# Kernel tuning notes

Hardware: AMD Instinct MI355X
Metric: run time of the kernel (lower is better)

## Reference

```python
import jax, jax.numpy as jnp
import numpy as np

B, C, H, W = 4, 256, 160, 160
N = 512
REID = 128
NUM_LAYERS = 2
BINS = 7          # adaptive_avg_pool2d target (7,7)
EPS_BN = 1e-5
EPS_NORM = 1e-12  # torch F.normalize eps


def setup_inputs() -> dict:
    key = jax.random.key(0)
    ks = jax.random.split(key, 8)
    x = jax.random.normal(ks[0], (B, C, H, W), jnp.float32)
    # valid normalized boxes: x1,y1 in [0,0.7], w,h in [0.1,0.3]
    xy1 = jax.random.uniform(ks[1], (B, N, 2), minval=0.0, maxval=0.7)
    wh = jax.random.uniform(ks[2], (B, N, 2), minval=0.1, maxval=0.3)
    bboxes = jnp.concatenate([xy1, jnp.minimum(xy1 + wh, 1.0)], axis=-1)
    # conv stack params (kaiming-ish init), BN in eval mode with running stats
    conv_w = jax.random.normal(ks[3], (NUM_LAYERS, C, C, 3, 3), jnp.float32) * np.sqrt(2.0 / (C * 9)).astype(np.float32)
    conv_b = jnp.zeros((NUM_LAYERS, C), jnp.float32)
    bn_gamma = jnp.ones((NUM_LAYERS, C), jnp.float32)
    bn_beta = jnp.zeros((NUM_LAYERS, C), jnp.float32)
    bn_mean = jnp.zeros((NUM_LAYERS, C), jnp.float32)
    bn_var = jnp.ones((NUM_LAYERS, C), jnp.float32)
    # reid_embedding MLP: Linear(C, C//2) -> ReLU -> Dropout(eval) -> Linear(C//2, REID)
    w1 = jax.random.normal(ks[4], (C // 2, C), jnp.float32) * 0.01
    b1 = jnp.zeros((C // 2,), jnp.float32)
    w2 = jax.random.normal(ks[5], (REID, C // 2), jnp.float32) * 0.01
    b2 = jnp.zeros((REID,), jnp.float32)
    return dict(x=x, bboxes=bboxes, conv_w=conv_w, conv_b=conv_b,
                bn_gamma=bn_gamma, bn_beta=bn_beta, bn_mean=bn_mean, bn_var=bn_var,
                w1=w1, b1=b1, w2=w2, b2=b2)


def _conv_bn_relu(x, w, b, gamma, beta, mean, var):
    y = jax.lax.conv_general_dilated(
        x, w, window_strides=(1, 1), padding=((1, 1), (1, 1)),
        dimension_numbers=('NCHW', 'OIHW', 'NCHW')) + b[None, :, None, None]
    scale = (gamma / jnp.sqrt(var + EPS_BN))[None, :, None, None]
    y = (y - mean[None, :, None, None]) * scale + beta[None, :, None, None]
    return jax.nn.relu(y)


def _roi_pool(S, box):
    # S: (C, H+1, W+1) integral image of the feature map; box: (4,) = x1,y1,x2,y2 in [0,1]
    x1 = jnp.clip(jnp.floor(box[0] * W).astype(jnp.int32), 0, W)
    y1 = jnp.clip(jnp.floor(box[1] * H).astype(jnp.int32), 0, H)
    x2 = jnp.clip(jnp.floor(box[2] * W).astype(jnp.int32), 0, W)
    y2 = jnp.clip(jnp.floor(box[3] * H).astype(jnp.int32), 0, H)
    valid = (x2 > x1) & (y2 > y1)
    hl = jnp.maximum(y2 - y1, 1)
    wl = jnp.maximum(x2 - x1, 1)
    i = jnp.arange(BINS)
    # PyTorch adaptive_avg_pool2d binning: [floor(i*L/B), ceil((i+1)*L/B))
    hs = y1 + (i * hl) // BINS
    he = y1 + ((i + 1) * hl + BINS - 1) // BINS
    ws = x1 + (i * wl) // BINS
    we = x1 + ((i + 1) * wl + BINS - 1) // BINS
    # bin sums via integral image -> (C, 7, 7)
    s = (S[:, he[:, None], we[None, :]] - S[:, hs[:, None], we[None, :]]
         - S[:, he[:, None], ws[None, :]] + S[:, hs[:, None], ws[None, :]])
    area = ((he - hs)[:, None] * (we - ws)[None, :]).astype(S.dtype)
    # adaptive 7x7 avg pool, then global avg pool over the 7x7 grid
    pooled = jnp.mean(s / area, axis=(1, 2))  # (C,)
    return pooled, valid


def reference(x, bboxes, conv_w, conv_b, bn_gamma, bn_beta, bn_mean, bn_var, w1, b1, w2, b2):
    f = x
    for l in range(NUM_LAYERS):
        f = _conv_bn_relu(f, conv_w[l], conv_b[l], bn_gamma[l], bn_beta[l], bn_mean[l], bn_var[l])
    # integral image, zero-padded: S[b,c,y,x] = sum of f[b,c,:y,:x] -> (B, C, H+1, W+1)
    S = jnp.pad(jnp.cumsum(jnp.cumsum(f, axis=2), axis=3), ((0, 0), (0, 0), (1, 0), (1, 0)))
    pooled, valid = jax.vmap(jax.vmap(_roi_pool, in_axes=(None, 0)), in_axes=(0, 0))(S, bboxes)
    # reid_embedding MLP (dropout is identity in eval)
    h = jax.nn.relu(jnp.einsum('bnc,hc->bnh', pooled, w1) + b1)
    feat = jnp.einsum('bnh,rh->bnr', h, w2) + b2
    feat = jnp.where(valid[..., None], feat, jnp.zeros((), feat.dtype))
    norm = jnp.maximum(jnp.linalg.norm(feat, axis=-1, keepdims=True), EPS_NORM)
    return feat / norm
```

## Files before the change

kernel.cpp:

```cpp
#include <hip/hip_runtime.h>
#include <hip/hip_bf16.h>

typedef __attribute__((ext_vector_type(8))) short s16x8;
typedef __attribute__((ext_vector_type(4))) float f32x4;


__device__ __forceinline__ void async_ld16(const void* g, void* l) {
  __builtin_amdgcn_global_load_lds(
      (const __attribute__((address_space(1))) void*)g,
      (__attribute__((address_space(3))) void*)l, 16, 0, 0);
}

__global__ __launch_bounds__(256) void zero_borders(__hip_bfloat16* __restrict__ xpad,
                                                    __hip_bfloat16* __restrict__ f1) {
  int bi = blockIdx.x;
  int buf = bi / 2576; int rem = bi - buf * 2576;
  int b = rem / 644;   int e = rem - b * 644;
  int y, x;
  if (e < 162)      { y = 0;           x = e; }
  else if (e < 324) { y = 161;         x = e - 162; }
  else if (e < 484) { y = e - 324 + 1; x = 0; }
  else              { y = e - 484 + 1; x = 161; }
  __hip_bfloat16* p = (buf ? f1 : xpad) + (((size_t)b * 162 + y) * 162 + x) * 256 + threadIdx.x;
  *p = __float2bfloat16(0.f);
}

__global__ __launch_bounds__(256) void nchw2nhwc(const float* __restrict__ x,
                                                 __hip_bfloat16* __restrict__ xpad) {
  __shared__ float tile[32][33];
  int blk = blockIdx.x;
  int xt = blk % 5;
  int ct = (blk / 5) & 7;
  int by = blk / 40;
  int b = by / 160, y = by - (by / 160) * 160;
  int tx = threadIdx.x, ty = threadIdx.y;
  const float* src = x + (((size_t)(b * 256 + ct * 32)) * 160 + y) * 160 + xt * 32 + tx;
#pragma unroll
  for (int k = 0; k < 4; k++) tile[ty * 4 + k][tx] = src[(size_t)(ty * 4 + k) * 25600];
  __syncthreads();
  __hip_bfloat16* dst = xpad + (((size_t)(b * 162 + y + 1)) * 162 + (xt * 32 + 1)) * 256 + ct * 32 + tx;
#pragma unroll
  for (int k = 0; k < 4; k++) {
    int xx = ty * 4 + k;
    dst[(size_t)xx * 256] = __float2bfloat16(tile[tx][xx]);
  }
}

__global__ __launch_bounds__(256) void pack_w(const float* __restrict__ cw,
                                              __hip_bfloat16* __restrict__ wpk) {
  int t = blockIdx.x * 256 + threadIdx.x;
  int ci = t & 255, co = (t >> 8) & 255, rest = t >> 16;
  int tap = rest % 9, l = rest / 9;
  int dy = tap / 3, dx = tap - dy * 3;
  float v = cw[((((size_t)l * 256 + co) * 256 + ci) * 3 + dy) * 3 + dx];
  wpk[(((size_t)l * 9 + tap) * 256 + co) * 256 + ci] = __float2bfloat16(v);
}

__global__ void prep_bn(const float* __restrict__ cb, const float* __restrict__ g,
                        const float* __restrict__ bt, const float* __restrict__ mn,
                        const float* __restrict__ vr, float* __restrict__ ab) {
  int t = blockIdx.x * 256 + threadIdx.x;
  float a = g[t] / sqrtf(vr[t] + 1e-5f);
  ab[t] = a;
  ab[512 + t] = (cb[t] - mn[t]) * a + bt[t];
}

__global__ __launch_bounds__(256) void pack_mlp(const float* __restrict__ w1,
                                                const float* __restrict__ w2,
                                                float* __restrict__ w1t,
                                                float* __restrict__ w2t) {
  int t = blockIdx.x * 256 + threadIdx.x;
  if (t < 32768) {
    int h = t >> 8, k = t & 255;
    w1t[k * 128 + h] = w1[h * 256 + k];
  } else {
    int u = t - 32768;
    int r = u >> 7, k = u & 127;
    w2t[k * 128 + r] = w2[r * 128 + k];
  }
}

__global__ __launch_bounds__(256, 2) void conv_bn_relu(
    const __hip_bfloat16* __restrict__ inp, __hip_bfloat16* __restrict__ outp,
    const __hip_bfloat16* __restrict__ wpk,
    const float* __restrict__ alpha, const float* __restrict__ beff) {
  __shared__ __align__(16) short As[2 * 128 * 64];
  __shared__ __align__(16) short Bs[2 * 128 * 64];
  const int t = threadIdx.x;
  const int logical = ((blockIdx.x & 7) * 200) + (blockIdx.x >> 3);
  const int mtile = logical >> 1;
  const int ntile = logical & 1;
  const int l = t & 63;
  const int wv = t >> 6;
  const int lr = l & 15, lq = l >> 4;
  const int wm = wv >> 1, wn = wv & 1;
  const int co0 = ntile << 7;

  const int srow = t >> 3;
  const int koff = (((t & 7) ^ (srow & 7)) << 3);
  const short* inS = (const short*)inp;
  const short* wS = (const short*)wpk;
  long abase[4];
#pragma unroll
  for (int i = 0; i < 4; i++) {
    int p = mtile * 128 + i * 32 + srow;
    int b = p / 25600; int r = p - b * 25600; int y = r / 160; int x = r - y * 160;
    abase[i] = (((long)b * 162 + y) * 162 + x) * 256 + koff;
  }
  const long bbase = ((long)(co0 + srow)) * 256 + koff;

  auto stage = [&](int u) {
    const int tap = u >> 2;
    const int dy = tap / 3, dx = tap - dy * 3;
    const long atap = ((long)(dy * 162 + dx)) * 256 + (long)(u & 3) * 64;
    const long btap = (long)tap * 65536 + (long)(u & 3) * 64;
    short* ad = As + ((u & 1) << 13) + t * 8;
    short* bd = Bs + ((u & 1) << 13) + t * 8;
#pragma unroll
    for (int i = 0; i < 4; i++) async_ld16(inS + abase[i] + atap, ad + i * 2048);
#pragma unroll
    for (int i = 0; i < 4; i++) async_ld16(wS + bbase + btap + i * 8192, bd + i * 2048);
  };

  f32x4 acc[4][4];
#pragma unroll
  for (int i = 0; i < 4; i++)
#pragma unroll
    for (int j = 0; j < 4; j++) acc[i][j] = (f32x4){0.f, 0.f, 0.f, 0.f};

  stage(0);
  __syncthreads();

#pragma unroll 1
  for (int u = 0; u < 36; ++u) {
    if (u < 35) stage(u + 1);
    const short* Ab = As + ((u & 1) << 13);
    const short* Bb = Bs + ((u & 1) << 13);
#pragma unroll
    for (int kk = 0; kk < 2; ++kk) {
      const int ps = (((kk << 2) | lq) ^ (lr & 7)) << 3;
      s16x8 av[4], bv[4];
#pragma unroll
      for (int mi = 0; mi < 4; ++mi)
        av[mi] = *(const s16x8*)&Ab[(wm * 64 + mi * 16 + lr) * 64 + ps];
#pragma unroll
      for (int ni = 0; ni < 4; ++ni)
        bv[ni] = *(const s16x8*)&Bb[(wn * 64 + ni * 16 + lr) * 64 + ps];
      __builtin_amdgcn_s_setprio(1);
#pragma unroll
      for (int mi = 0; mi < 4; ++mi)
#pragma unroll
        for (int ni = 0; ni < 4; ++ni)
          acc[mi][ni] = __builtin_amdgcn_mfma_f32_16x16x32_bf16(av[mi], bv[ni], acc[mi][ni], 0, 0, 0);
      __builtin_amdgcn_s_setprio(0);
    }
    __syncthreads();
  }

  float al[4], be_[4];
#pragma unroll
  for (int ni = 0; ni < 4; ++ni) {
    int co = co0 + wn * 64 + ni * 16 + lr;
    al[ni] = alpha[co];
    be_[ni] = beff[co];
  }
#pragma unroll
  for (int mi = 0; mi < 4; ++mi) {
    int prow = mtile * 128 + wm * 64 + mi * 16 + lq * 4;
#pragma unroll
    for (int j = 0; j < 4; ++j) {
      int p = prow + j;
      int b = p / 25600; int r = p - b * 25600; int y = r / 160; int x = r - y * 160;
      long ob = (((long)b * 162 + (y + 1)) * 162 + (x + 1)) * 256 + co0 + wn * 64;
#pragma unroll
      for (int ni = 0; ni < 4; ++ni) {
        float v = acc[mi][ni][j] * al[ni] + be_[ni];
        outp[ob + ni * 16 + lr] = __float2bfloat16(fmaxf(v, 0.f));
      }
    }
  }
}

__global__ __launch_bounds__(256) void cumsum_w(const __hip_bfloat16* __restrict__ f2,
                                                float* __restrict__ S) {
  int row = blockIdx.x * 2 + (threadIdx.x >> 7);
  int b = row / 160, y = row - (row / 160) * 160;
  int cp = threadIdx.x & 127;
  const unsigned* src =
      (const unsigned*)((const short*)f2 + (((size_t)b * 162 + y + 1) * 162 + 1) * 256) + cp;
  float2* dst = (float2*)(S + (((size_t)b * 161 + y + 1) * 161) * 256) + cp;
  dst[0] = float2{0.f, 0.f};
  float r0 = 0.f, r1 = 0.f;
  for (int x4 = 0; x4 < 160; x4 += 4) {
    unsigned v[4];
#pragma unroll
    for (int k = 0; k < 4; k++) v[k] = src[(size_t)(x4 + k) * 128];
#pragma unroll
    for (int k = 0; k < 4; k++) {
      r0 += __uint_as_float((v[k] & 0xffffu) << 16);
      r1 += __uint_as_float(v[k] & 0xffff0000u);
      dst[(size_t)(x4 + k + 1) * 128] = float2{r0, r1};
    }
  }
}

__global__ __launch_bounds__(256) void cumsum_h(float* __restrict__ S) {
  int bi = blockIdx.x;
  int b = bi / 161, q = bi - (bi / 161) * 161;
  int c = threadIdx.x;
  float* col = S + (((size_t)b * 161) * 161 + q) * 256 + c;
  const size_t ys = (size_t)161 * 256;
  col[0] = 0.f;
  float run = 0.f;
  for (int y0 = 1; y0 <= 160; y0 += 8) {
    float v[8];
#pragma unroll
    for (int k = 0; k < 8; k++) v[k] = col[(size_t)(y0 + k) * ys];
#pragma unroll
    for (int k = 0; k < 8; k++) { run += v[k]; col[(size_t)(y0 + k) * ys] = run; }
  }
}

__global__ __launch_bounds__(256) void roi_pool(const float* __restrict__ S,
                                                const float* __restrict__ bbox,
                                                float* __restrict__ pooled,
                                                int* __restrict__ valid) {
  int bn = blockIdx.x;
  int b = bn >> 9;
  int c = threadIdx.x;
  float bx1 = bbox[bn * 4 + 0], by1 = bbox[bn * 4 + 1];
  float bx2 = bbox[bn * 4 + 2], by2 = bbox[bn * 4 + 3];
  int x1 = min(max((int)floorf(bx1 * 160.f), 0), 160);
  int y1 = min(max((int)floorf(by1 * 160.f), 0), 160);
  int x2 = min(max((int)floorf(bx2 * 160.f), 0), 160);
  int y2 = min(max((int)floorf(by2 * 160.f), 0), 160);
  int vld = (x2 > x1 && y2 > y1) ? 1 : 0;
  int hl = max(y2 - y1, 1), wl = max(x2 - x1, 1);
  int hs[7], he[7], ws_[7], we_[7];
  float rh[7], rw[7];
#pragma unroll
  for (int i = 0; i < 7; i++) {
    hs[i] = y1 + (i * hl) / 7;
    he[i] = y1 + ((i + 1) * hl + 6) / 7;
    rh[i] = 1.f / (float)(he[i] - hs[i]);
    ws_[i] = x1 + (i * wl) / 7;
    we_[i] = x1 + ((i + 1) * wl + 6) / 7;
    rw[i] = 1.f / (float)(we_[i] - ws_[i]);
  }
  const float* Sb = S + (size_t)b * 161 * 161 * 256 + c;
  float acc = 0.f;
#pragma unroll
  for (int i = 0; i < 7; i++) {
    const float* rE = Sb + (size_t)he[i] * (161 * 256);
    const float* rS = Sb + (size_t)hs[i] * (161 * 256);
#pragma unroll
    for (int j = 0; j < 7; j++) {
      size_t qe = (size_t)we_[j] * 256, qs = (size_t)ws_[j] * 256;
      float s = rE[qe] - rS[qe] - rE[qs] + rS[qs];
      acc += s * (rh[i] * rw[j]);
    }
  }
  pooled[(size_t)bn * 256 + c] = acc * (1.f / 49.f);
  if (c == 0) valid[bn] = vld;
}

__global__ __launch_bounds__(128) void mlp_norm(const float* __restrict__ pooled,
                                                const int* __restrict__ valid,
                                                const float* __restrict__ w1t,
                                                const float* __restrict__ b1,
                                                const float* __restrict__ w2t,
                                                const float* __restrict__ b2,
                                                float* __restrict__ out) {
  int bn = blockIdx.x;
  int t = threadIdx.x;
  __shared__ float pl[256];
  __shared__ float hh[128];
  __shared__ float red[2];
  pl[t] = pooled[(size_t)bn * 256 + t];
  pl[t + 128] = pooled[(size_t)bn * 256 + 128 + t];
  __syncthreads();
  float a = b1[t];
#pragma unroll 8
  for (int k = 0; k < 256; k++) a += w1t[k * 128 + t] * pl[k];
  hh[t] = fmaxf(a, 0.f);
  __syncthreads();
  float f = b2[t];
#pragma unroll 8
  for (int k = 0; k < 128; k++) f += w2t[k * 128 + t] * hh[k];
  if (!valid[bn]) f = 0.f;
  float ss = f * f;
#pragma unroll
  for (int off = 32; off > 0; off >>= 1) ss += __shfl_xor(ss, off);
  if ((t & 63) == 0) red[t >> 6] = ss;
  __syncthreads();
  float nrm = fmaxf(sqrtf(red[0] + red[1]), 1e-12f);
  out[(size_t)bn * 128 + t] = f / nrm;
}

extern "C" void kernel_launch(void* const* d_in, const int* in_sizes, int n_in,
                              void* d_out, int out_size, void* d_ws, size_t ws_size,
                              hipStream_t stream) {
  const float* x = (const float*)d_in[0];
  const float* bboxes = (const float*)d_in[1];
  const float* conv_w = (const float*)d_in[2];
  const float* conv_b = (const float*)d_in[3];
  const float* bn_g = (const float*)d_in[4];
  const float* bn_b = (const float*)d_in[5];
  const float* bn_m = (const float*)d_in[6];
  const float* bn_v = (const float*)d_in[7];
  const float* w1 = (const float*)d_in[8];
  const float* b1 = (const float*)d_in[9];
  const float* w2 = (const float*)d_in[10];
  const float* b2 = (const float*)d_in[11];

  char* ws = (char*)d_ws;
  const size_t PADB = (size_t)4 * 162 * 162 * 256 * 2;
  const size_t WPKB = (size_t)2 * 9 * 256 * 256 * 2;
  const size_t SB = (size_t)4 * 161 * 161 * 256 * 4;
  const size_t PLB = (size_t)4 * 512 * 256 * 4;

  __hip_bfloat16* xpad = (__hip_bfloat16*)(ws);
  __hip_bfloat16* f1 = (__hip_bfloat16*)(ws + PADB);
  __hip_bfloat16* wpk = (__hip_bfloat16*)(ws + 2 * PADB);
  float* abuf = (float*)(ws + 2 * PADB + WPKB);
  float* S = (float*)(ws + 2 * PADB + WPKB + 4096);
  float* pooled = (float*)(ws + 2 * PADB + WPKB + 4096 + SB);
  int* valid = (int*)(ws + 2 * PADB + WPKB + 4096 + SB + PLB);
  float* w1t = (float*)(ws + 2 * PADB + WPKB + 4096 + SB + PLB + 8192);
  float* w2t = w1t + 32768;

  zero_borders<<<5152, 256, 0, stream>>>(xpad, f1);
  nchw2nhwc<<<25600, dim3(32, 8), 0, stream>>>(x, xpad);
  pack_w<<<4608, 256, 0, stream>>>(conv_w, wpk);
  prep_bn<<<2, 256, 0, stream>>>(conv_b, bn_g, bn_b, bn_m, bn_v, abuf);
  pack_mlp<<<192, 256, 0, stream>>>(w1, w2, w1t, w2t);

  conv_bn_relu<<<1600, 256, 0, stream>>>(xpad, f1, wpk, abuf, abuf + 512);
  conv_bn_relu<<<1600, 256, 0, stream>>>(f1, xpad, wpk + (size_t)9 * 256 * 256, abuf + 256, abuf + 768);

  cumsum_w<<<320, 256, 0, stream>>>(xpad, S);
  cumsum_h<<<644, 256, 0, stream>>>(S);
  roi_pool<<<2048, 256, 0, stream>>>(S, bboxes, pooled, valid);
  mlp_norm<<<2048, 128, 0, stream>>>(pooled, valid, w1t, b1, w2t, b2, (float*)d_out);
}
```

Measured before the change: 459.7 us.

## Use 4-stage K=32 async LDS pipeline with vmcnt-based waits in conv GEMM

Restructures the implicit-GEMM conv main loop from a double-buffered K=64 stage (36 iterations, full syncthreads) to a 4-buffer ring of K=32 stages (72 iterations) with three stages in flight. Waits use explicit s_waitcnt vmcnt plus a single barrier per iteration instead of waiting for all loads, so global-to-LDS latency is hidden further ahead. The LDS swizzle and per-thread load mapping change to match the 32-wide rows. Total LDS stays the same, but there are twice as many barriers and MFMA work per barrier is halved.

```diff
diff --git a/kernel.cpp b/kernel.cpp
--- a/kernel.cpp
+++ b/kernel.cpp
@@ -84,8 +84,8 @@
     const __hip_bfloat16* __restrict__ inp, __hip_bfloat16* __restrict__ outp,
     const __hip_bfloat16* __restrict__ wpk,
     const float* __restrict__ alpha, const float* __restrict__ beff) {
-  __shared__ __align__(16) short As[2 * 128 * 64];
-  __shared__ __align__(16) short Bs[2 * 128 * 64];
+  __shared__ __align__(16) short As[4 * 4096];
+  __shared__ __align__(16) short Bs[4 * 4096];
   const int t = threadIdx.x;
   const int logical = ((blockIdx.x & 7) * 200) + (blockIdx.x >> 3);
   const int mtile = logical >> 1;
@@ -96,30 +96,32 @@
   const int wm = wv >> 1, wn = wv & 1;
   const int co0 = ntile << 7;
 
-  const int srow = t >> 3;
-  const int koff = (((t & 7) ^ (srow & 7)) << 3);
+  const int koff = (((t & 3) ^ ((t >> 3) & 3)) << 3);
   const short* inS = (const short*)inp;
   const short* wS = (const short*)wpk;
-  long abase[4];
-#pragma unroll
-  for (int i = 0; i < 4; i++) {
-    int p = mtile * 128 + i * 32 + srow;
-    int b = p / 25600; int r = p - b * 25600; int y = r / 160; int x = r - y * 160;
-    abase[i] = (((long)b * 162 + y) * 162 + x) * 256 + koff;
-  }
-  const long bbase = ((long)(co0 + srow)) * 256 + koff;
+  long abase0, abase1;
+  {
+    int p0 = mtile * 128 + (t >> 2);
+    int b0 = p0 / 25600; int r0 = p0 - b0 * 25600; int y0 = r0 / 160; int x0 = r0 - y0 * 160;
+    abase0 = (((long)b0 * 162 + y0) * 162 + x0) * 256 + koff;
+    int p1 = p0 + 64;
+    int b1 = p1 / 25600; int r1 = p1 - b1 * 25600; int y1 = r1 / 160; int x1 = r1 - y1 * 160;
+    abase1 = (((long)b1 * 162 + y1) * 162 + x1) * 256 + koff;
+  }
+  const long bbase0 = ((long)(co0 + (t >> 2))) * 256 + koff;
+  const long bbase1 = bbase0 + 64 * 256;
 
   auto stage = [&](int u) {
-    const int tap = u >> 2;
+    const int tap = u >> 3, kc = u & 7;
     const int dy = tap / 3, dx = tap - dy * 3;
-    const long atap = ((long)(dy * 162 + dx)) * 256 + (long)(u & 3) * 64;
-    const long btap = (long)tap * 65536 + (long)(u & 3) * 64;
-    short* ad = As + ((u & 1) << 13) + t * 8;
-    short* bd = Bs + ((u & 1) << 13) + t * 8;
-#pragma unroll
-    for (int i = 0; i < 4; i++) async_ld16(inS + abase[i] + atap, ad + i * 2048);
-#pragma unroll
-    for (int i = 0; i < 4; i++) async_ld16(wS + bbase + btap + i * 8192, bd + i * 2048);
+    const long aoff = ((long)(dy * 162 + dx)) * 256 + kc * 32;
+    const long boff = (long)tap * 65536 + kc * 32;
+    short* ad = As + (u & 3) * 4096 + t * 8;
+    short* bd = Bs + (u & 3) * 4096 + t * 8;
+    async_ld16(inS + abase0 + aoff, ad);
+    async_ld16(inS + abase1 + aoff, ad + 2048);
+    async_ld16(wS + bbase0 + boff, bd);
+    async_ld16(wS + bbase1 + boff, bd + 2048);
   };
 
   f32x4 acc[4][4];
@@ -128,34 +130,48 @@
 #pragma unroll
     for (int j = 0; j < 4; j++) acc[i][j] = (f32x4){0.f, 0.f, 0.f, 0.f};
 
-  stage(0);
-  __syncthreads();
-
+  const int psA = ((lq ^ ((lr >> 1) & 3)) << 3);
+
+  auto compute = [&](int u) {
+    const short* Ab = As + (u & 3) * 4096;
+    const short* Bb = Bs + (u & 3) * 4096;
+    s16x8 av[4], bv[4];
+#pragma unroll
+    for (int mi = 0; mi < 4; ++mi)
+      av[mi] = *(const s16x8*)&Ab[(wm * 64 + mi * 16 + lr) * 32 + psA];
+#pragma unroll
+    for (int ni = 0; ni < 4; ++ni)
+      bv[ni] = *(const s16x8*)&Bb[(wn * 64 + ni * 16 + lr) * 32 + psA];
+    __builtin_amdgcn_s_setprio(1);
+#pragma unroll
+    for (int mi = 0; mi < 4; ++mi)
+#pragma unroll
+      for (int ni = 0; ni < 4; ++ni)
+        acc[mi][ni] = __builtin_amdgcn_mfma_f32_16x16x32_bf16(av[mi], bv[ni], acc[mi][ni], 0, 0, 0);
+    __builtin_amdgcn_s_setprio(0);
+  };
+
+  stage(0); stage(1); stage(2);
 #pragma unroll 1
-  for (int u = 0; u < 36; ++u) {
-    if (u < 35) stage(u + 1);
-    const short* Ab = As + ((u & 1) << 13);
-    const short* Bb = Bs + ((u & 1) << 13);
-#pragma unroll
-    for (int kk = 0; kk < 2; ++kk) {
-      const int ps = (((kk << 2) | lq) ^ (lr & 7)) << 3;
-      s16x8 av[4], bv[4];
-#pragma unroll
-      for (int mi = 0; mi < 4; ++mi)
-        av[mi] = *(const s16x8*)&Ab[(wm * 64 + mi * 16 + lr) * 64 + ps];
-#pragma unroll
-      for (int ni = 0; ni < 4; ++ni)
-        bv[ni] = *(const s16x8*)&Bb[(wn * 64 + ni * 16 + lr) * 64 + ps];
-      __builtin_amdgcn_s_setprio(1);
-#pragma unroll
-      for (int mi = 0; mi < 4; ++mi)
-#pragma unroll
-        for (int ni = 0; ni < 4; ++ni)
-          acc[mi][ni] = __builtin_amdgcn_mfma_f32_16x16x32_bf16(av[mi], bv[ni], acc[mi][ni], 0, 0, 0);
-      __builtin_amdgcn_s_setprio(0);
-    }
-    __syncthreads();
-  }
+  for (int u = 0; u < 69; ++u) {
+    asm volatile("s_waitcnt vmcnt(8)" ::: "memory");
+    __builtin_amdgcn_s_barrier();
+    __builtin_amdgcn_sched_barrier(0);
+    stage(u + 3);
+    compute(u);
+  }
+  asm volatile("s_waitcnt vmcnt(8)" ::: "memory");
+  __builtin_amdgcn_s_barrier();
+  __builtin_amdgcn_sched_barrier(0);
+  compute(69);
+  asm volatile("s_waitcnt vmcnt(4)" ::: "memory");
+  __builtin_amdgcn_s_barrier();
+  __builtin_amdgcn_sched_barrier(0);
+  compute(70);
+  asm volatile("s_waitcnt vmcnt(0)" ::: "memory");
+  __builtin_amdgcn_s_barrier();
+  __builtin_amdgcn_sched_barrier(0);
+  compute(71);
 
   float al[4], be_[4];
 #pragma unroll
```

After: 517.4 us. 1.13x slower.

## Widen conv tile to all 256 output channels and drop LDS double buffering

Applied to the files above, without the earlier changes.

The implicit-GEMM conv now computes all 256 output channels per block (128x256 tile, 8 MFMA column tiles per wave), halving the grid to 800 blocks so each activation tile is loaded from global memory once instead of twice. The double-buffered prefetch is replaced by a single buffer with barriers before and after each load stage. Load and compute therefore no longer overlap within a block, and the doubled accumulator count raises register pressure, which may lower occupancy below the declared two blocks per CU.

```diff
diff --git a/kernel.cpp b/kernel.cpp
--- a/kernel.cpp
+++ b/kernel.cpp
@@ -84,17 +84,14 @@
     const __hip_bfloat16* __restrict__ inp, __hip_bfloat16* __restrict__ outp,
     const __hip_bfloat16* __restrict__ wpk,
     const float* __restrict__ alpha, const float* __restrict__ beff) {
-  __shared__ __align__(16) short As[2 * 128 * 64];
-  __shared__ __align__(16) short Bs[2 * 128 * 64];
+  __shared__ __align__(16) short As[128 * 64];
+  __shared__ __align__(16) short Bs[256 * 64];
   const int t = threadIdx.x;
-  const int logical = ((blockIdx.x & 7) * 200) + (blockIdx.x >> 3);
-  const int mtile = logical >> 1;
-  const int ntile = logical & 1;
+  const int mtile = ((blockIdx.x & 7) * 100) + (blockIdx.x >> 3);
   const int l = t & 63;
   const int wv = t >> 6;
   const int lr = l & 15, lq = l >> 4;
   const int wm = wv >> 1, wn = wv & 1;
-  const int co0 = ntile << 7;
 
   const int srow = t >> 3;
   const int koff = (((t & 7) ^ (srow & 7)) << 3);
@@ -107,60 +104,52 @@
     int b = p / 25600; int r = p - b * 25600; int y = r / 160; int x = r - y * 160;
     abase[i] = (((long)b * 162 + y) * 162 + x) * 256 + koff;
   }
-  const long bbase = ((long)(co0 + srow)) * 256 + koff;
-
-  auto stage = [&](int u) {
-    const int tap = u >> 2;
-    const int dy = tap / 3, dx = tap - dy * 3;
-    const long atap = ((long)(dy * 162 + dx)) * 256 + (long)(u & 3) * 64;
-    const long btap = (long)tap * 65536 + (long)(u & 3) * 64;
-    short* ad = As + ((u & 1) << 13) + t * 8;
-    short* bd = Bs + ((u & 1) << 13) + t * 8;
-#pragma unroll
-    for (int i = 0; i < 4; i++) async_ld16(inS + abase[i] + atap, ad + i * 2048);
-#pragma unroll
-    for (int i = 0; i < 4; i++) async_ld16(wS + bbase + btap + i * 8192, bd + i * 2048);
-  };
-
-  f32x4 acc[4][4];
+  const long bbase = ((long)srow) * 256 + koff;
+
+  f32x4 acc[4][8];
 #pragma unroll
   for (int i = 0; i < 4; i++)
 #pragma unroll
-    for (int j = 0; j < 4; j++) acc[i][j] = (f32x4){0.f, 0.f, 0.f, 0.f};
-
-  stage(0);
-  __syncthreads();
+    for (int j = 0; j < 8; j++) acc[i][j] = (f32x4){0.f, 0.f, 0.f, 0.f};
 
 #pragma unroll 1
   for (int u = 0; u < 36; ++u) {
-    if (u < 35) stage(u + 1);
-    const short* Ab = As + ((u & 1) << 13);
-    const short* Bb = Bs + ((u & 1) << 13);
+    const int tap = u >> 2, kc = u & 3;
+    const int dy = tap / 3, dx = tap - dy * 3;
+    const long aoff = ((long)(dy * 162 + dx)) * 256 + kc * 64;
+    const long boff = (long)tap * 65536 + kc * 64;
+    __syncthreads();
+#pragma unroll
+    for (int i = 0; i < 4; i++)
+      async_ld16(inS + abase[i] + aoff, As + i * 2048 + t * 8);
+#pragma unroll
+    for (int j = 0; j < 8; j++)
+      async_ld16(wS + bbase + boff + (long)j * 8192, Bs + j * 2048 + t * 8);
+    __syncthreads();
 #pragma unroll
     for (int kk = 0; kk < 2; ++kk) {
       const int ps = (((kk << 2) | lq) ^ (lr & 7)) << 3;
-      s16x8 av[4], bv[4];
+      s16x8 av[4], bv[8];
 #pragma unroll
       for (int mi = 0; mi < 4; ++mi)
-        av[mi] = *(const s16x8*)&Ab[(wm * 64 + mi * 16 + lr) * 64 + ps];
-#pragma unroll
-      for (int ni = 0; ni < 4; ++ni)
-        bv[ni] = *(const s16x8*)&Bb[(wn * 64 + ni * 16 + lr) * 64 + ps];
+        av[mi] = *(const s16x8*)&As[(wm * 64 + mi * 16 + lr) * 64 + ps];
+#pragma unroll
+      for (int ni = 0; ni < 8; ++ni)
+        bv[ni] = *(const s16x8*)&Bs[(wn * 128 + ni * 16 + lr) * 64 + ps];
       __builtin_amdgcn_s_setprio(1);
 #pragma unroll
       for (int mi = 0; mi < 4; ++mi)
 #pragma unroll
-        for (int ni = 0; ni < 4; ++ni)
+        for (int ni = 0; ni < 8; ++ni)
           acc[mi][ni] = __builtin_amdgcn_mfma_f32_16x16x32_bf16(av[mi], bv[ni], acc[mi][ni], 0, 0, 0);
       __builtin_amdgcn_s_setprio(0);
     }
-    __syncthreads();
-  }
-
-  float al[4], be_[4];
-#pragma unroll
-  for (int ni = 0; ni < 4; ++ni) {
-    int co = co0 + wn * 64 + ni * 16 + lr;
+  }
+
+  float al[8], be_[8];
+#pragma unroll
+  for (int ni = 0; ni < 8; ++ni) {
+    int co = wn * 128 + ni * 16 + lr;
     al[ni] = alpha[co];
     be_[ni] = beff[co];
   }
@@ -171,9 +160,9 @@
     for (int j = 0; j < 4; ++j) {
       int p = prow + j;
       int b = p / 25600; int r = p - b * 25600; int y = r / 160; int x = r - y * 160;
-      long ob = (((long)b * 162 + (y + 1)) * 162 + (x + 1)) * 256 + co0 + wn * 64;
-#pragma unroll
-      for (int ni = 0; ni < 4; ++ni) {
+      long ob = (((long)b * 162 + (y + 1)) * 162 + (x + 1)) * 256 + wn * 128;
+#pragma unroll
+      for (int ni = 0; ni < 8; ++ni) {
         float v = acc[mi][ni][j] * al[ni] + be_[ni];
         outp[ob + ni * 16 + lr] = __float2bfloat16(fmaxf(v, 0.f));
       }
@@ -335,8 +324,8 @@
   prep_bn<<<2, 256, 0, stream>>>(conv_b, bn_g, bn_b, bn_m, bn_v, abuf);
   pack_mlp<<<192, 256, 0, stream>>>(w1, w2, w1t, w2t);
 
-  conv_bn_relu<<<1600, 256, 0, stream>>>(xpad, f1, wpk, abuf, abuf + 512);
-  conv_bn_relu<<<1600, 256, 0, stream>>>(f1, xpad, wpk + (size_t)9 * 256 * 256, abuf + 256, abuf + 768);
+  conv_bn_relu<<<800, 256, 0, stream>>>(xpad, f1, wpk, abuf, abuf + 512);
+  conv_bn_relu<<<800, 256, 0, stream>>>(f1, xpad, wpk + (size_t)9 * 256 * 256, abuf + 256, abuf + 768);
 
   cumsum_w<<<320, 256, 0, stream>>>(xpad, S);
   cumsum_h<<<644, 256, 0, stream>>>(S);
```

New measurement: 403.9 us. -12.1%, faster.

## Enlarge conv GEMM tile to 256x256 with 512-thread blocks

Applied to the files above, without the earlier changes.

The implicit-GEMM conv kernel now has each block cover 256 output pixels by all 256 output channels, using 8 waves that each compute a 128x64 sub-tile. The N-tile split is removed, and the grid shrinks from 1600 to 400 blocks. The aim is more MFMA work per LDS fragment read and per staged input, and no duplicate loads of the A tile across two channel halves. The cost is a doubled LDS footprint (128KB per block), likely one block per CU, more accumulator registers, and a coarser grid that may leave CUs idle in the last round.

```diff
diff --git a/kernel.cpp b/kernel.cpp
--- a/kernel.cpp
+++ b/kernel.cpp
@@ -80,21 +80,18 @@
   }
 }
 
-__global__ __launch_bounds__(256, 2) void conv_bn_relu(
+__global__ __launch_bounds__(512, 2) void conv_bn_relu(
     const __hip_bfloat16* __restrict__ inp, __hip_bfloat16* __restrict__ outp,
     const __hip_bfloat16* __restrict__ wpk,
     const float* __restrict__ alpha, const float* __restrict__ beff) {
-  __shared__ __align__(16) short As[2 * 128 * 64];
-  __shared__ __align__(16) short Bs[2 * 128 * 64];
+  __shared__ __align__(16) short As[2 * 256 * 64];
+  __shared__ __align__(16) short Bs[2 * 256 * 64];
   const int t = threadIdx.x;
-  const int logical = ((blockIdx.x & 7) * 200) + (blockIdx.x >> 3);
-  const int mtile = logical >> 1;
-  const int ntile = logical & 1;
+  const int mtile = ((blockIdx.x & 7) * 50) + (blockIdx.x >> 3);
   const int l = t & 63;
   const int wv = t >> 6;
   const int lr = l & 15, lq = l >> 4;
-  const int wm = wv >> 1, wn = wv & 1;
-  const int co0 = ntile << 7;
+  const int wm = wv >> 2, wn = wv & 3;
 
   const int srow = t >> 3;
   const int koff = (((t & 7) ^ (srow & 7)) << 3);
@@ -103,52 +100,54 @@
   long abase[4];
 #pragma unroll
   for (int i = 0; i < 4; i++) {
-    int p = mtile * 128 + i * 32 + srow;
+    int p = mtile * 256 + i * 64 + srow;
     int b = p / 25600; int r = p - b * 25600; int y = r / 160; int x = r - y * 160;
     abase[i] = (((long)b * 162 + y) * 162 + x) * 256 + koff;
   }
-  const long bbase = ((long)(co0 + srow)) * 256 + koff;
-
-  auto stage = [&](int u) {
-    const int tap = u >> 2;
+  const long bbase = ((long)srow) * 256 + koff;
+
+  auto stage = [&](int v) {
+    const int tap = v >> 2, kc = v & 3;
     const int dy = tap / 3, dx = tap - dy * 3;
-    const long atap = ((long)(dy * 162 + dx)) * 256 + (long)(u & 3) * 64;
-    const long btap = (long)tap * 65536 + (long)(u & 3) * 64;
-    short* ad = As + ((u & 1) << 13) + t * 8;
-    short* bd = Bs + ((u & 1) << 13) + t * 8;
-#pragma unroll
-    for (int i = 0; i < 4; i++) async_ld16(inS + abase[i] + atap, ad + i * 2048);
-#pragma unroll
-    for (int i = 0; i < 4; i++) async_ld16(wS + bbase + btap + i * 8192, bd + i * 2048);
+    const long aoff = ((long)(dy * 162 + dx)) * 256 + kc * 64;
+    const long boff = (long)tap * 65536 + kc * 64;
+    short* ad = As + (v & 1) * 16384 + t * 8;
+    short* bd = Bs + (v & 1) * 16384 + t * 8;
+#pragma unroll
+    for (int i = 0; i < 4; i++)
+      async_ld16(inS + abase[i] + aoff, ad + i * 4096);
+#pragma unroll
+    for (int i = 0; i < 4; i++)
+      async_ld16(wS + bbase + boff + (long)i * 16384, bd + i * 4096);
   };
 
-  f32x4 acc[4][4];
-#pragma unroll
-  for (int i = 0; i < 4; i++)
+  f32x4 acc[8][4];
+#pragma unroll
+  for (int i = 0; i < 8; i++)
 #pragma unroll
     for (int j = 0; j < 4; j++) acc[i][j] = (f32x4){0.f, 0.f, 0.f, 0.f};
 
   stage(0);
   __syncthreads();
 
-#pragma unroll 1
+#pragma unroll 2
   for (int u = 0; u < 36; ++u) {
     if (u < 35) stage(u + 1);
-    const short* Ab = As + ((u & 1) << 13);
-    const short* Bb = Bs + ((u & 1) << 13);
+    const short* Ab = As + (u & 1) * 16384;
+    const short* Bb = Bs + (u & 1) * 16384;
 #pragma unroll
     for (int kk = 0; kk < 2; ++kk) {
       const int ps = (((kk << 2) | lq) ^ (lr & 7)) << 3;
-      s16x8 av[4], bv[4];
-#pragma unroll
-      for (int mi = 0; mi < 4; ++mi)
-        av[mi] = *(const s16x8*)&Ab[(wm * 64 + mi * 16 + lr) * 64 + ps];
+      s16x8 av[8], bv[4];
+#pragma unroll
+      for (int mi = 0; mi < 8; ++mi)
+        av[mi] = *(const s16x8*)&Ab[(wm * 128 + mi * 16 + lr) * 64 + ps];
 #pragma unroll
       for (int ni = 0; ni < 4; ++ni)
         bv[ni] = *(const s16x8*)&Bb[(wn * 64 + ni * 16 + lr) * 64 + ps];
       __builtin_amdgcn_s_setprio(1);
 #pragma unroll
-      for (int mi = 0; mi < 4; ++mi)
+      for (int mi = 0; mi < 8; ++mi)
 #pragma unroll
         for (int ni = 0; ni < 4; ++ni)
           acc[mi][ni] = __builtin_amdgcn_mfma_f32_16x16x32_bf16(av[mi], bv[ni], acc[mi][ni], 0, 0, 0);
@@ -160,18 +159,18 @@
   float al[4], be_[4];
 #pragma unroll
   for (int ni = 0; ni < 4; ++ni) {
-    int co = co0 + wn * 64 + ni * 16 + lr;
+    int co = wn * 64 + ni * 16 + lr;
     al[ni] = alpha[co];
     be_[ni] = beff[co];
   }
 #pragma unroll
-  for (int mi = 0; mi < 4; ++mi) {
-    int prow = mtile * 128 + wm * 64 + mi * 16 + lq * 4;
+  for (int mi = 0; mi < 8; ++mi) {
+    int prow = mtile * 256 + wm * 128 + mi * 16 + lq * 4;
 #pragma unroll
     for (int j = 0; j < 4; ++j) {
       int p = prow + j;
       int b = p / 25600; int r = p - b * 25600; int y = r / 160; int x = r - y * 160;
-      long ob = (((long)b * 162 + (y + 1)) * 162 + (x + 1)) * 256 + co0 + wn * 64;
+      long ob = (((long)b * 162 + (y + 1)) * 162 + (x + 1)) * 256 + wn * 64;
 #pragma unroll
       for (int ni = 0; ni < 4; ++ni) {
         float v = acc[mi][ni][j] * al[ni] + be_[ni];
@@ -335,8 +334,8 @@
   prep_bn<<<2, 256, 0, stream>>>(conv_b, bn_g, bn_b, bn_m, bn_v, abuf);
   pack_mlp<<<192, 256, 0, stream>>>(w1, w2, w1t, w2t);
 
-  conv_bn_relu<<<1600, 256, 0, stream>>>(xpad, f1, wpk, abuf, abuf + 512);
-  conv_bn_relu<<<1600, 256, 0, stream>>>(f1, xpad, wpk + (size_t)9 * 256 * 256, abuf + 256, abuf + 768);
+  conv_bn_relu<<<400, 512, 0, stream>>>(xpad, f1, wpk, abuf, abuf + 512);
+  conv_bn_relu<<<400, 512, 0, stream>>>(f1, xpad, wpk + (size_t)9 * 256 * 256, abuf + 256, abuf + 768);
 
   cumsum_w<<<320, 256, 0, stream>>>(xpad, S);
   cumsum_h<<<644, 256, 0, stream>>>(S);
```

Result: faster. 445.1 us (-3.2%).
